# Optimization experiments

Measured on AMD Instinct MI355X. Metric: run time of the kernel, lower is better.

## Reference

```python
import jax, jax.numpy as jnp
import numpy as np

B, S, HID = 2, 2048, 2048
H, HK, D = 16, 4, 128  # num_heads, num_kv_heads, head_dim
G = H // HK            # GQA group size


def _make_rope(B, S, D):
    pos = jnp.arange(S, dtype=jnp.float32)
    inv_freq = 1.0 / (10000.0 ** (jnp.arange(0, D, 2, dtype=jnp.float32) / D))
    freqs = pos[:, None] * inv_freq[None, :]          # [S, D/2]
    emb = jnp.concatenate([freqs, freqs], axis=-1)     # [S, D]
    cos = jnp.broadcast_to(jnp.cos(emb)[None], (B, S, D))
    sin = jnp.broadcast_to(jnp.sin(emb)[None], (B, S, D))
    return cos, sin


def setup_inputs() -> dict:
    key = jax.random.key(0)
    k0, k1, k2 = jax.random.split(key, 3)
    hidden_states = jax.random.normal(k0, (B, S, HID), dtype=jnp.float32)
    cos, sin = _make_rope(B, S, D)
    w_qkv = jax.random.normal(k1, ((H + 2 * HK) * D, HID), dtype=jnp.float32) * 0.02
    b_qkv = jnp.zeros(((H + 2 * HK) * D,), dtype=jnp.float32)
    w_o = jax.random.normal(k2, (HID, HID), dtype=jnp.float32) * 0.02
    b_o = jnp.zeros((HID,), dtype=jnp.float32)
    return {"hidden_states": hidden_states, "cos": cos, "sin": sin,
            "w_qkv": w_qkv, "b_qkv": b_qkv, "w_o": w_o, "b_o": b_o}


def _rotate_half(x):
    x1, x2 = jnp.split(x, 2, axis=-1)
    return jnp.concatenate([-x2, x1], axis=-1)


def reference(hidden_states, cos, sin, w_qkv, b_qkv, w_o, b_o):
    b, s, _ = hidden_states.shape
    qkv = jnp.einsum('bsh,oh->bso', hidden_states, w_qkv) + b_qkv
    q, k, v = jnp.split(qkv, [H * D, (H + HK) * D], axis=-1)
    # [B, heads, S, D]
    q = q.reshape(b, s, H, D).transpose(0, 2, 1, 3)
    k = k.reshape(b, s, HK, D).transpose(0, 2, 1, 3)
    v = v.reshape(b, s, HK, D).transpose(0, 2, 1, 3)
    # RoPE (cos/sin broadcast over head axis)
    c = cos[:, None, :, :]
    sn = sin[:, None, :, :]
    q = q * c + _rotate_half(q) * sn
    k = k * c + _rotate_half(k) * sn
    # GQA attention without materializing repeated K/V: group q heads
    qg = q.reshape(b, HK, G, s, D)
    scale = 1.0 / jnp.sqrt(jnp.float32(D))
    scores = jnp.einsum('bkgqd,bkpd->bkgqp', qg, k) * scale  # [B,HK,G,S,S]
    probs = jax.nn.softmax(scores, axis=-1)
    out = jnp.einsum('bkgqp,bkpd->bkgqd', probs, v)           # [B,HK,G,S,D]
    out = out.reshape(b, H, s, D).transpose(0, 2, 1, 3).reshape(b, s, H * D)
    return jnp.einsum('bsh,oh->bso', out, w_o) + b_o
```

## Files before the change

kernel.cpp:

```cpp
#include <hip/hip_runtime.h>
#include <hip/hip_bf16.h>
#include <stdint.h>

typedef __bf16 bf16x8 __attribute__((ext_vector_type(8)));
typedef float f32x4 __attribute__((ext_vector_type(4)));
typedef float f32x16 __attribute__((ext_vector_type(16)));
typedef float f32x4v __attribute__((ext_vector_type(4)));
typedef unsigned short u16;
typedef unsigned int u32;
typedef u16 u16x8 __attribute__((ext_vector_type(8)));
typedef u32 u32x4 __attribute__((ext_vector_type(4)));

#define B_ 2
#define S_ 2048
#define HID_ 2048
#define H_ 16
#define HK_ 4
#define D_ 128
#define NQKV_ 3072

__device__ __forceinline__ u16 f2bf(float f) {
  u32 u = __builtin_bit_cast(u32, f);
  u32 r = (u + 0x7fffu + ((u >> 16) & 1u)) >> 16;
  return (u16)r;
}
__device__ __forceinline__ float bf2f(u16 v) {
  u32 u = ((u32)v) << 16;
  return __builtin_bit_cast(float, u);
}
__device__ __forceinline__ u32 cvtpk(float lo, float hi) {
  u32 r;
  asm("v_cvt_pk_bf16_f32 %0, %1, %2" : "=v"(r) : "v"(lo), "v"(hi));
  return r;
}
__device__ __forceinline__ void gload_lds16(const void* g, void* l) {
  __builtin_amdgcn_global_load_lds((const __attribute__((address_space(1))) void*)g,
                                   (__attribute__((address_space(3))) void*)l, 16, 0, 0);
}

__global__ __launch_bounds__(256) void k_cvt3(const float* __restrict__ a, u16* __restrict__ oa, int na,
                                              const float* __restrict__ b, u16* __restrict__ ob, int nb,
                                              const float* __restrict__ c, u16* __restrict__ oc, int nc) {
  int total = na + nb + nc;
  for (int i = blockIdx.x * 256 + threadIdx.x; i < total; i += gridDim.x * 256) {
    const float* src;
    u16* dst;
    int j = i;
    if (j < na) { src = a; dst = oa; }
    else if (j < na + nb) { j -= na; src = b; dst = ob; }
    else { j -= na + nb; src = c; dst = oc; }
    const f32x4v* p = (const f32x4v*)(src + (size_t)j * 8);
    f32x4v x = p[0], y = p[1];
    u16x8 w;
    w[0] = f2bf(x[0]); w[1] = f2bf(x[1]); w[2] = f2bf(x[2]); w[3] = f2bf(x[3]);
    w[4] = f2bf(y[0]); w[5] = f2bf(y[1]); w[6] = f2bf(y[2]); w[7] = f2bf(y[3]);
    *(u16x8*)(dst + (size_t)j * 8) = w;
  }
}

template <int ISSUES>
__device__ __forceinline__ void stage_half(const u16* __restrict__ src, int K, char* ldsb, int tid) {
#pragma unroll
  for (int i = 0; i < ISSUES; ++i) {
    int off = i * 8192 + tid * 16;
    int r = off >> 7, cb = off & 127;
    int scb = cb ^ ((r & 7) << 4);
    gload_lds16((const char*)(src + (size_t)r * K) + scb, ldsb + i * 8192 + (tid & ~63) * 16);
  }
}

template <int BM, typename CT>
__global__ __launch_bounds__(512, 1) void k_gemm8p(const u16* __restrict__ A, const u16* __restrict__ Bm,
                                                   const float* __restrict__ bias, CT* __restrict__ C,
                                                   int M, int N, int K) {
  constexpr int HAR = BM / 2;
  constexpr int AHB = HAR * 128;
  constexpr int AISS = AHB / 8192;
  constexpr int MREP = BM / 32;
  constexpr int MQ = MREP / 4;
  constexpr int DB = 2 * AHB + 32768;
  __shared__ __attribute__((aligned(16))) char lds[2 * DB];
  const int tid = threadIdx.x, lane = tid & 63;
  const int wid = tid >> 6, wm = wid >> 2, wn = wid & 3;
  const int l15 = lane & 15, l4 = lane >> 4;
  const int nwg = gridDim.x * gridDim.y;
  const int bid = blockIdx.y * gridDim.x + blockIdx.x;
  const int wgid = (bid & 7) * (nwg >> 3) + (bid >> 3);
  const int bx = wgid % gridDim.x, by = wgid / gridDim.x;
  const int row0 = by * BM, col0 = bx * 256;
  const int NT = K >> 6;

  f32x4 acc[MREP][4] = {};

  auto stageA = [&](int t, int h) {
    stage_half<AISS>(A + (size_t)(row0 + h * HAR) * K + t * 64, K, lds + (t & 1) * DB + h * AHB, tid);
  };
  auto stageB = [&](int t, int h) {
    stage_half<2>(Bm + (size_t)(col0 + h * 128) * K + t * 64, K, lds + (t & 1) * DB + 2 * AHB + h * 16384, tid);
  };

  stageA(0, 0); stageA(0, 1); stageB(0, 0); stageB(0, 1);
  if (NT > 1) { stageB(1, 0); stageB(1, 1); }
  if (NT > 1) asm volatile("s_waitcnt vmcnt(4)" ::: "memory");
  else        asm volatile("s_waitcnt vmcnt(0)" ::: "memory");
  __builtin_amdgcn_s_barrier();

  const char* myA = lds + wm * AHB;
  const char* myB = lds + 2 * AHB + (wn >> 1) * 16384;
  const int rBb = (wn & 1) * 64;

  for (int t = 0; t < NT; ++t) {
    const int d = t & 1;
    const char* Ab = myA + d * DB;
    const char* Bb = myB + d * DB;
    bf16x8 bfr[4][2];
#pragma unroll
    for (int j = 0; j < 4; ++j) {
      if (j == 0) {
#pragma unroll
        for (int n = 0; n < 4; ++n)
#pragma unroll
          for (int ks = 0; ks < 2; ++ks) {
            int r = rBb + n * 16 + l15;
            bfr[n][ks] = *(const bf16x8*)(Bb + r * 128 + ((ks * 64 + l4 * 16) ^ ((r & 7) << 4)));
          }
      }
      bf16x8 afr[MQ][2];
#pragma unroll
      for (int mq = 0; mq < MQ; ++mq)
#pragma unroll
        for (int ks = 0; ks < 2; ++ks) {
          int r = (j * MQ + mq) * 16 + l15;
          afr[mq][ks] = *(const bf16x8*)(Ab + r * 128 + ((ks * 64 + l4 * 16) ^ ((r & 7) << 4)));
        }
      if (j == 0) { if (t + 1 < NT) stageA(t + 1, 0); }
      else if (j == 1) { if (t + 1 < NT) stageA(t + 1, 1); }
      else if (j == 2) { if (t + 2 < NT) stageB(t + 2, 0); }
      else {
        if (t + 2 < NT) { stageB(t + 2, 1); asm volatile("s_waitcnt vmcnt(4)" ::: "memory"); }
        else             asm volatile("s_waitcnt vmcnt(0)" ::: "memory");
      }
      __builtin_amdgcn_s_barrier();
      asm volatile("s_waitcnt lgkmcnt(0)" ::: "memory");
      __builtin_amdgcn_s_setprio(1);
#pragma unroll
      for (int mq = 0; mq < MQ; ++mq)
#pragma unroll
        for (int ks = 0; ks < 2; ++ks)
#pragma unroll
          for (int n = 0; n < 4; ++n)
            acc[j * MQ + mq][n] =
                __builtin_amdgcn_mfma_f32_16x16x32_bf16(afr[mq][ks], bfr[n][ks], acc[j * MQ + mq][n], 0, 0, 0);
      __builtin_amdgcn_s_setprio(0);
      __builtin_amdgcn_s_barrier();
    }
  }

#pragma unroll
  for (int m = 0; m < MREP; ++m) {
    int grow = row0 + wm * HAR + m * 16 + l4 * 4;
#pragma unroll
    for (int n = 0; n < 4; ++n) {
      int gcol = col0 + wn * 64 + n * 16 + l15;
      float bv = bias[gcol];
#pragma unroll
      for (int r2 = 0; r2 < 4; ++r2) {
        float v = acc[m][n][r2] + bv;
        if constexpr (sizeof(CT) == 2) C[(size_t)(grow + r2) * N + gcol] = (CT)f2bf(v);
        else                           C[(size_t)(grow + r2) * N + gcol] = v;
      }
    }
  }
}

__global__ __launch_bounds__(256) void k_rope_split(const u16* __restrict__ qkv,
                                                    const float* __restrict__ cosb,
                                                    const float* __restrict__ sinb,
                                                    u16* __restrict__ Qb, u16* __restrict__ Kb,
                                                    u16* __restrict__ Vt) {
  const int bs = blockIdx.x;
  const int b = bs >> 11, s = bs & 2047;
  const size_t base = (size_t)bs * NQKV_;
  const size_t cs = (size_t)bs * D_;
  const int tid = threadIdx.x;
  const float qscale = 0.08838834764831845f;

  if (tid < 160) {
    const bool isq = tid < 128;
    const int idx = isq ? tid : (tid - 128);
    const int hh = idx >> 3, d0 = (idx & 7) * 8;
    const size_t srcb = base + (isq ? 0 : H_ * D_) + hh * D_;
    bf16x8 x1 = *(const bf16x8*)(qkv + srcb + d0);
    bf16x8 x2 = *(const bf16x8*)(qkv + srcb + d0 + 64);
    u16x8 y1, y2;
    const u16x8 u1 = __builtin_bit_cast(u16x8, x1);
    const u16x8 u2 = __builtin_bit_cast(u16x8, x2);
    const float sc = isq ? qscale : 1.0f;
#pragma unroll
    for (int i = 0; i < 8; ++i) {
      float f1 = bf2f(u1[i]), f2 = bf2f(u2[i]);
      float c1 = cosb[cs + d0 + i], s1 = sinb[cs + d0 + i];
      float c2 = cosb[cs + 64 + d0 + i], s2 = sinb[cs + 64 + d0 + i];
      y1[i] = f2bf((f1 * c1 - f2 * s1) * sc);
      y2[i] = f2bf((f2 * c2 + f1 * s2) * sc);
    }
    size_t o;
    if (isq) o = ((size_t)(b * H_ + hh) * S_ + s) * D_ + d0;
    else     o = ((size_t)(b * HK_ + hh) * S_ + s) * D_ + d0;
    u16* dst = isq ? Qb : Kb;
    *(u16x8*)(dst + o) = y1;
    *(u16x8*)(dst + o + 64) = y2;
  } else if (tid < 224) {
    const int idx = tid - 160;
    const int hk = idx >> 4, d0 = (idx & 15) * 8;
    bf16x8 xv = *(const bf16x8*)(qkv + base + (H_ + HK_) * D_ + hk * D_ + d0);
    const u16x8 uv = __builtin_bit_cast(u16x8, xv);
    u16* vb = Vt + (size_t)(b * HK_ + hk) * D_ * S_ + s;
#pragma unroll
    for (int i = 0; i < 8; ++i) vb[(size_t)(d0 + i) * S_] = uv[i];
  }
}

__global__ __launch_bounds__(512, 2) void k_attn(const u16* __restrict__ Qb, const u16* __restrict__ Kb,
                                                 const u16* __restrict__ Vt, u16* __restrict__ Ob) {
  __shared__ __attribute__((aligned(16))) char lds[65536];
  const int qt = blockIdx.x;
  const int bh = blockIdx.y;
  const int b = bh >> 4, h = bh & 15, hk = h >> 2;
  const int tid = threadIdx.x, lane = tid & 63, wid = tid >> 6;
  const int l31 = lane & 31, hi = lane >> 5;

  const int qrow = qt * 256 + wid * 32 + l31;
  const u16* qptr = Qb + ((size_t)(b * H_ + h) * S_ + qrow) * D_;
  bf16x8 qf[8];
#pragma unroll
  for (int ks = 0; ks < 8; ++ks) qf[ks] = *(const bf16x8*)(qptr + ks * 16 + hi * 8);

  const u16* kbase = Kb + (size_t)(b * HK_ + hk) * S_ * D_;
  const u16* vbase = Vt + (size_t)(b * HK_ + hk) * D_ * S_;

  int krow[2], kc[2], vrow[2], vc[2];
#pragma unroll
  for (int i = 0; i < 2; ++i) {
    int s = tid + i * 512;
    krow[i] = s >> 4; kc[i] = s & 15;
    vrow[i] = s >> 3; vc[i] = s & 7;
  }

  f32x16 o[4] = {};
  float mrun = -1e30f, lrun = 0.f;

  bf16x8 kreg[2], vreg[2];
#pragma unroll
  for (int i = 0; i < 2; ++i) {
    kreg[i] = *(const bf16x8*)(kbase + (size_t)krow[i] * D_ + kc[i] * 8);
    vreg[i] = *(const bf16x8*)(vbase + (size_t)vrow[i] * S_ + vc[i] * 8);
  }
#pragma unroll
  for (int i = 0; i < 2; ++i) {
    *(bf16x8*)(lds + ((krow[i] * 256 + kc[i] * 16) ^ ((krow[i] & 15) << 4))) = kreg[i];
    *(bf16x8*)(lds + 16384 + ((vrow[i] * 128 + vc[i] * 16) ^ ((vrow[i] & 7) << 4))) = vreg[i];
  }
  __syncthreads();

  for (int kt = 0; kt < 32; ++kt) {
    const int cur = kt & 1;
    const char* lKc = lds + cur * 32768;
    const char* lVc = lKc + 16384;

    if (kt < 31) {
#pragma unroll
      for (int i = 0; i < 2; ++i) {
        kreg[i] = *(const bf16x8*)(kbase + (size_t)((kt + 1) * 64 + krow[i]) * D_ + kc[i] * 8);
        vreg[i] = *(const bf16x8*)(vbase + (size_t)vrow[i] * S_ + (kt + 1) * 64 + vc[i] * 8);
      }
    }

    f32x16 sc[2] = {};
    __builtin_amdgcn_s_setprio(1);
#pragma unroll
    for (int ks = 0; ks < 8; ++ks) {
#pragma unroll
      for (int T = 0; T < 2; ++T) {
        int row = T * 32 + l31;
        bf16x8 kf = *(const bf16x8*)(lKc + ((row * 256 + ks * 32 + hi * 16) ^ ((row & 15) << 4)));
        sc[T] = __builtin_amdgcn_mfma_f32_32x32x16_bf16(kf, qf[ks], sc[T], 0, 0, 0);
      }
    }
    __builtin_amdgcn_s_setprio(0);

    float pmax = sc[0][0];
#pragma unroll
    for (int r = 1; r < 16; ++r) pmax = fmaxf(pmax, sc[0][r]);
#pragma unroll
    for (int r = 0; r < 16; ++r) pmax = fmaxf(pmax, sc[1][r]);
    pmax = fmaxf(pmax, __shfl_xor(pmax, 32));
    if (__any(pmax > mrun + 8.f)) {
      float mn = fmaxf(mrun, pmax);
      float alpha = __expf(mrun - mn);
      mrun = mn;
      lrun *= alpha;
#pragma unroll
      for (int dt = 0; dt < 4; ++dt)
#pragma unroll
        for (int r = 0; r < 16; ++r) o[dt][r] *= alpha;
    }
    float rs = 0.f;
#pragma unroll
    for (int T = 0; T < 2; ++T)
#pragma unroll
      for (int r = 0; r < 16; ++r) {
        float p = __expf(sc[T][r] - mrun);
        sc[T][r] = p;
        rs += p;
      }
    rs += __shfl_xor(rs, 32);
    lrun += rs;

    bf16x8 pf[4];
#pragma unroll
    for (int T = 0; T < 2; ++T) {
#pragma unroll
      for (int g = 0; g < 2; ++g) {
        u32 a0 = cvtpk(sc[T][8 * g + 0], sc[T][8 * g + 1]);
        u32 a1 = cvtpk(sc[T][8 * g + 2], sc[T][8 * g + 3]);
        u32 a2 = cvtpk(sc[T][8 * g + 4], sc[T][8 * g + 5]);
        u32 a3 = cvtpk(sc[T][8 * g + 6], sc[T][8 * g + 7]);
        u32 x0 = (u32)__shfl_xor((int)a0, 32);
        u32 x1 = (u32)__shfl_xor((int)a1, 32);
        u32 x2 = (u32)__shfl_xor((int)a2, 32);
        u32 x3 = (u32)__shfl_xor((int)a3, 32);
        u32 s0 = hi ? x2 : a0;
        u32 s1 = hi ? x3 : a1;
        u32 s2 = hi ? a2 : x0;
        u32 s3 = hi ? a3 : x1;
        u32x4 w = {s0, s1, s2, s3};
        pf[T * 2 + g] = __builtin_bit_cast(bf16x8, w);
      }
    }

    __builtin_amdgcn_s_setprio(1);
#pragma unroll
    for (int ks2 = 0; ks2 < 4; ++ks2) {
#pragma unroll
      for (int dt = 0; dt < 4; ++dt) {
        int row = dt * 32 + l31;
        bf16x8 vf = *(const bf16x8*)(lVc + ((row * 128 + ks2 * 32 + hi * 16) ^ ((row & 7) << 4)));
        o[dt] = __builtin_amdgcn_mfma_f32_32x32x16_bf16(vf, pf[ks2], o[dt], 0, 0, 0);
      }
    }
    __builtin_amdgcn_s_setprio(0);

    if (kt < 31) {
      char* nK = lds + (cur ^ 1) * 32768;
      char* nV = nK + 16384;
#pragma unroll
      for (int i = 0; i < 2; ++i) {
        *(bf16x8*)(nK + ((krow[i] * 256 + kc[i] * 16) ^ ((krow[i] & 15) << 4))) = kreg[i];
        *(bf16x8*)(nV + ((vrow[i] * 128 + vc[i] * 16) ^ ((vrow[i] & 7) << 4))) = vreg[i];
      }
    }
    __syncthreads();
  }

  float inv = 1.0f / lrun;
  char* myreg = lds + wid * 8192;
#pragma unroll
  for (int dt = 0; dt < 4; ++dt)
#pragma unroll
    for (int t = 0; t < 8; ++t) {
      u32 w = cvtpk(o[dt][2 * t] * inv, o[dt][2 * t + 1] * inv);
      int d0 = dt * 32 + 2 * (t & 1) + 8 * (t >> 1) + 4 * hi;
      *(u32*)(myreg + ((l31 * 256 + d0 * 2) ^ ((l31 & 15) << 4))) = w;
    }
  asm volatile("s_waitcnt lgkmcnt(0)");
  {
    int q = lane >> 1, hf = lane & 1;
    int srow = qt * 256 + wid * 32 + q;
    u16* orow = Ob + ((size_t)(b * S_ + srow)) * HID_ + h * 128 + hf * 64;
#pragma unroll
    for (int i = 0; i < 8; ++i) {
      bf16x8 vv = *(const bf16x8*)(myreg + ((q * 256 + hf * 128 + i * 16) ^ ((q & 15) << 4)));
      *(bf16x8*)(orow + i * 8) = vv;
    }
  }
}

extern "C" void kernel_launch(void* const* d_in, const int* in_sizes, int n_in,
                              void* d_out, int out_size, void* d_ws, size_t ws_size,
                              hipStream_t stream) {
  const float* hs = (const float*)d_in[0];
  const float* cosb = (const float*)d_in[1];
  const float* sinb = (const float*)d_in[2];
  const float* w_qkv = (const float*)d_in[3];
  const float* b_qkv = (const float*)d_in[4];
  const float* w_o = (const float*)d_in[5];
  const float* b_o = (const float*)d_in[6];
  float* out = (float*)d_out;

  char* ws = (char*)d_ws;
  u16* Xb    = (u16*)ws;
  u16* Wqkvb = (u16*)(ws + 16777216);
  u16* Wob   = (u16*)(ws + 29360128);
  u16* qkvb  = (u16*)(ws + 37748736);
  u16* Qb    = (u16*)(ws + 62914560);
  u16* Kb    = (u16*)(ws + 79691776);
  u16* Vt    = (u16*)(ws + 83886080);
  u16* Ob = Xb;

  hipLaunchKernelGGL(k_cvt3, dim3(2048), dim3(256), 0, stream,
                     hs, Xb, (B_ * S_ * HID_) / 8,
                     w_qkv, Wqkvb, (NQKV_ * HID_) / 8,
                     w_o, Wob, (HID_ * HID_) / 8);
  hipLaunchKernelGGL((k_gemm8p<256, u16>), dim3(NQKV_ / 256, (B_ * S_) / 256), dim3(512), 0, stream,
                     Xb, Wqkvb, b_qkv, qkvb, B_ * S_, NQKV_, HID_);
  hipLaunchKernelGGL(k_rope_split, dim3(B_ * S_), dim3(256), 0, stream, qkvb, cosb, sinb, Qb, Kb, Vt);
  hipLaunchKernelGGL(k_attn, dim3(S_ / 256, B_ * H_), dim3(512), 0, stream, Qb, Kb, Vt, Ob);
  hipLaunchKernelGGL((k_gemm8p<128, float>), dim3(HID_ / 256, (B_ * S_) / 128), dim3(512), 0, stream,
                     Ob, Wob, b_o, out, B_ * S_, HID_, HID_);
}
```

Baseline: 217.6 us.

## Split attention KV sequence across two wave groups and merge partial softmax states

Each attention block now covers 128 query rows instead of 256, and its two groups of four waves each process half of the KV sequence. The partial outputs and running max/sum are combined through LDS at the end. K/V tiles are loaded directly into LDS with gload_lds16 instead of going through registers. This doubles the grid (512 blocks) for better CU occupancy, but each group is now single-buffered, adds two barriers per iteration, and adds an LDS merge step.

```diff
diff --git a/kernel.cpp b/kernel.cpp
--- a/kernel.cpp
+++ b/kernel.cpp
@@ -223,59 +223,51 @@
 
 __global__ __launch_bounds__(512, 2) void k_attn(const u16* __restrict__ Qb, const u16* __restrict__ Kb,
                                                  const u16* __restrict__ Vt, u16* __restrict__ Ob) {
-  __shared__ __attribute__((aligned(16))) char lds[65536];
+  __shared__ __attribute__((aligned(16))) char lds[66560];
   const int qt = blockIdx.x;
   const int bh = blockIdx.y;
   const int b = bh >> 4, h = bh & 15, hk = h >> 2;
   const int tid = threadIdx.x, lane = tid & 63, wid = tid >> 6;
   const int l31 = lane & 31, hi = lane >> 5;
-
-  const int qrow = qt * 256 + wid * 32 + l31;
+  const int g = wid >> 2, wq = wid & 3;
+
+  const int qrow = qt * 128 + wq * 32 + l31;
   const u16* qptr = Qb + ((size_t)(b * H_ + h) * S_ + qrow) * D_;
   bf16x8 qf[8];
 #pragma unroll
   for (int ks = 0; ks < 8; ++ks) qf[ks] = *(const bf16x8*)(qptr + ks * 16 + hi * 8);
 
-  const u16* kbase = Kb + (size_t)(b * HK_ + hk) * S_ * D_;
-  const u16* vbase = Vt + (size_t)(b * HK_ + hk) * D_ * S_;
-
-  int krow[2], kc[2], vrow[2], vc[2];
-#pragma unroll
-  for (int i = 0; i < 2; ++i) {
-    int s = tid + i * 512;
-    krow[i] = s >> 4; kc[i] = s & 15;
-    vrow[i] = s >> 3; vc[i] = s & 7;
-  }
+  const char* kB = (const char*)(Kb + (size_t)(b * HK_ + hk) * S_ * D_);
+  const char* vB = (const char*)(Vt + (size_t)(b * HK_ + hk) * D_ * S_);
+  char* gbase = lds + g * 32768;
+
+  int koff[4], voff[4];
+#pragma unroll
+  for (int i = 0; i < 4; ++i) {
+    int c = wq * 256 + i * 64 + lane;
+    int row = c >> 4, u = c & 15;
+    koff[i] = row * 256 + ((u ^ (row & 15)) << 4);
+    int d = c >> 3, uv = c & 7;
+    voff[i] = d * (S_ * 2) + ((uv ^ (d & 7)) << 4);
+  }
+
+  auto stage = [&](int tt) {
+#pragma unroll
+    for (int i = 0; i < 4; ++i)
+      gload_lds16(kB + (size_t)tt * 16384 + koff[i], gbase + wq * 4096 + i * 1024);
+#pragma unroll
+    for (int i = 0; i < 4; ++i)
+      gload_lds16(vB + (size_t)tt * 128 + voff[i], gbase + 16384 + wq * 4096 + i * 1024);
+  };
 
   f32x16 o[4] = {};
   float mrun = -1e30f, lrun = 0.f;
 
-  bf16x8 kreg[2], vreg[2];
-#pragma unroll
-  for (int i = 0; i < 2; ++i) {
-    kreg[i] = *(const bf16x8*)(kbase + (size_t)krow[i] * D_ + kc[i] * 8);
-    vreg[i] = *(const bf16x8*)(vbase + (size_t)vrow[i] * S_ + vc[i] * 8);
-  }
-#pragma unroll
-  for (int i = 0; i < 2; ++i) {
-    *(bf16x8*)(lds + ((krow[i] * 256 + kc[i] * 16) ^ ((krow[i] & 15) << 4))) = kreg[i];
-    *(bf16x8*)(lds + 16384 + ((vrow[i] * 128 + vc[i] * 16) ^ ((vrow[i] & 7) << 4))) = vreg[i];
-  }
+  const int tt0 = g * 16;
+  stage(tt0);
   __syncthreads();
 
-  for (int kt = 0; kt < 32; ++kt) {
-    const int cur = kt & 1;
-    const char* lKc = lds + cur * 32768;
-    const char* lVc = lKc + 16384;
-
-    if (kt < 31) {
-#pragma unroll
-      for (int i = 0; i < 2; ++i) {
-        kreg[i] = *(const bf16x8*)(kbase + (size_t)((kt + 1) * 64 + krow[i]) * D_ + kc[i] * 8);
-        vreg[i] = *(const bf16x8*)(vbase + (size_t)vrow[i] * S_ + (kt + 1) * 64 + vc[i] * 8);
-      }
-    }
-
+  for (int t = 0; t < 16; ++t) {
     f32x16 sc[2] = {};
     __builtin_amdgcn_s_setprio(1);
 #pragma unroll
@@ -283,7 +275,7 @@
 #pragma unroll
       for (int T = 0; T < 2; ++T) {
         int row = T * 32 + l31;
-        bf16x8 kf = *(const bf16x8*)(lKc + ((row * 256 + ks * 32 + hi * 16) ^ ((row & 15) << 4)));
+        bf16x8 kf = *(const bf16x8*)(gbase + ((row * 256 + ks * 32 + hi * 16) ^ ((row & 15) << 4)));
         sc[T] = __builtin_amdgcn_mfma_f32_32x32x16_bf16(kf, qf[ks], sc[T], 0, 0, 0);
       }
     }
@@ -321,11 +313,11 @@
 #pragma unroll
     for (int T = 0; T < 2; ++T) {
 #pragma unroll
-      for (int g = 0; g < 2; ++g) {
-        u32 a0 = cvtpk(sc[T][8 * g + 0], sc[T][8 * g + 1]);
-        u32 a1 = cvtpk(sc[T][8 * g + 2], sc[T][8 * g + 3]);
-        u32 a2 = cvtpk(sc[T][8 * g + 4], sc[T][8 * g + 5]);
-        u32 a3 = cvtpk(sc[T][8 * g + 6], sc[T][8 * g + 7]);
+      for (int gg = 0; gg < 2; ++gg) {
+        u32 a0 = cvtpk(sc[T][8 * gg + 0], sc[T][8 * gg + 1]);
+        u32 a1 = cvtpk(sc[T][8 * gg + 2], sc[T][8 * gg + 3]);
+        u32 a2 = cvtpk(sc[T][8 * gg + 4], sc[T][8 * gg + 5]);
+        u32 a3 = cvtpk(sc[T][8 * gg + 6], sc[T][8 * gg + 7]);
         u32 x0 = (u32)__shfl_xor((int)a0, 32);
         u32 x1 = (u32)__shfl_xor((int)a1, 32);
         u32 x2 = (u32)__shfl_xor((int)a2, 32);
@@ -335,7 +327,7 @@
         u32 s2 = hi ? a2 : x0;
         u32 s3 = hi ? a3 : x1;
         u32x4 w = {s0, s1, s2, s3};
-        pf[T * 2 + g] = __builtin_bit_cast(bf16x8, w);
+        pf[T * 2 + gg] = __builtin_bit_cast(bf16x8, w);
       }
     }
 
@@ -345,43 +337,69 @@
 #pragma unroll
       for (int dt = 0; dt < 4; ++dt) {
         int row = dt * 32 + l31;
-        bf16x8 vf = *(const bf16x8*)(lVc + ((row * 128 + ks2 * 32 + hi * 16) ^ ((row & 7) << 4)));
+        bf16x8 vf = *(const bf16x8*)(gbase + 16384 + ((row * 128 + ks2 * 32 + hi * 16) ^ ((row & 7) << 4)));
         o[dt] = __builtin_amdgcn_mfma_f32_32x32x16_bf16(vf, pf[ks2], o[dt], 0, 0, 0);
       }
     }
     __builtin_amdgcn_s_setprio(0);
 
-    if (kt < 31) {
-      char* nK = lds + (cur ^ 1) * 32768;
-      char* nV = nK + 16384;
-#pragma unroll
-      for (int i = 0; i < 2; ++i) {
-        *(bf16x8*)(nK + ((krow[i] * 256 + kc[i] * 16) ^ ((krow[i] & 15) << 4))) = kreg[i];
-        *(bf16x8*)(nV + ((vrow[i] * 128 + vc[i] * 16) ^ ((vrow[i] & 7) << 4))) = vreg[i];
-      }
-    }
     __syncthreads();
-  }
-
-  float inv = 1.0f / lrun;
-  char* myreg = lds + wid * 8192;
-#pragma unroll
-  for (int dt = 0; dt < 4; ++dt)
-#pragma unroll
-    for (int t = 0; t < 8; ++t) {
-      u32 w = cvtpk(o[dt][2 * t] * inv, o[dt][2 * t + 1] * inv);
-      int d0 = dt * 32 + 2 * (t & 1) + 8 * (t >> 1) + 4 * hi;
-      *(u32*)(myreg + ((l31 * 256 + d0 * 2) ^ ((l31 & 15) << 4))) = w;
-    }
-  asm volatile("s_waitcnt lgkmcnt(0)");
-  {
-    int q = lane >> 1, hf = lane & 1;
-    int srow = qt * 256 + wid * 32 + q;
-    u16* orow = Ob + ((size_t)(b * S_ + srow)) * HID_ + h * 128 + hf * 64;
-#pragma unroll
-    for (int i = 0; i < 8; ++i) {
-      bf16x8 vv = *(const bf16x8*)(myreg + ((q * 256 + hf * 128 + i * 16) ^ ((q & 15) << 4)));
-      *(bf16x8*)(orow + i * 8) = vv;
+    if (t < 15) stage(tt0 + t + 1);
+    __syncthreads();
+  }
+
+  float2* mlb = (float2*)(lds + 65536);
+  if (g == 1) {
+    char* ob = lds + wq * 16384;
+#pragma unroll
+    for (int dt = 0; dt < 4; ++dt)
+#pragma unroll
+      for (int r = 0; r < 4; ++r) {
+        f32x4 w = {o[dt][4 * r + 0], o[dt][4 * r + 1], o[dt][4 * r + 2], o[dt][4 * r + 3]};
+        *(f32x4*)(ob + ((size_t)((dt * 4 + r) * 64 + lane)) * 16) = w;
+      }
+    if (!hi) mlb[wq * 32 + l31] = float2{mrun, lrun};
+  }
+  __syncthreads();
+  float inv = 0.f;
+  if (g == 0) {
+    float2 ml1 = mlb[wq * 32 + l31];
+    float m = fmaxf(mrun, ml1.x);
+    float a0 = __expf(mrun - m), a1 = __expf(ml1.x - m);
+    float lt = lrun * a0 + ml1.y * a1;
+    char* ob = lds + wq * 16384;
+#pragma unroll
+    for (int dt = 0; dt < 4; ++dt)
+#pragma unroll
+      for (int r = 0; r < 4; ++r) {
+        f32x4 c1 = *(const f32x4*)(ob + ((size_t)((dt * 4 + r) * 64 + lane)) * 16);
+#pragma unroll
+        for (int j = 0; j < 4; ++j) o[dt][4 * r + j] = o[dt][4 * r + j] * a0 + c1[j] * a1;
+      }
+    inv = 1.0f / lt;
+  }
+  __syncthreads();
+
+  if (g == 0) {
+    char* myreg = lds + wq * 8192;
+#pragma unroll
+    for (int dt = 0; dt < 4; ++dt)
+#pragma unroll
+      for (int t = 0; t < 8; ++t) {
+        u32 w = cvtpk(o[dt][2 * t] * inv, o[dt][2 * t + 1] * inv);
+        int d0 = dt * 32 + 2 * (t & 1) + 8 * (t >> 1) + 4 * hi;
+        *(u32*)(myreg + ((l31 * 256 + d0 * 2) ^ ((l31 & 15) << 4))) = w;
+      }
+    asm volatile("s_waitcnt lgkmcnt(0)");
+    {
+      int q = lane >> 1, hf = lane & 1;
+      int srow = qt * 128 + wq * 32 + q;
+      u16* orow = Ob + ((size_t)(b * S_ + srow)) * HID_ + h * 128 + hf * 64;
+#pragma unroll
+      for (int i = 0; i < 8; ++i) {
+        bf16x8 vv = *(const bf16x8*)(myreg + ((q * 256 + hf * 128 + i * 16) ^ ((q & 15) << 4)));
+        *(bf16x8*)(orow + i * 8) = vv;
+      }
     }
   }
 }
@@ -415,7 +433,7 @@
   hipLaunchKernelGGL((k_gemm8p<256, u16>), dim3(NQKV_ / 256, (B_ * S_) / 256), dim3(512), 0, stream,
                      Xb, Wqkvb, b_qkv, qkvb, B_ * S_, NQKV_, HID_);
   hipLaunchKernelGGL(k_rope_split, dim3(B_ * S_), dim3(256), 0, stream, qkvb, cosb, sinb, Qb, Kb, Vt);
-  hipLaunchKernelGGL(k_attn, dim3(S_ / 256, B_ * H_), dim3(512), 0, stream, Qb, Kb, Vt, Ob);
+  hipLaunchKernelGGL(k_attn, dim3(S_ / 128, B_ * H_), dim3(512), 0, stream, Qb, Kb, Vt, Ob);
   hipLaunchKernelGGL((k_gemm8p<128, float>), dim3(HID_ / 256, (B_ * S_) / 128), dim3(512), 0, stream,
                      Ob, Wob, b_o, out, B_ * S_, HID_, HID_);
 }
```

Measured after the change: 232.0 us. 1.07x slower.

## Fuse RoPE and Q/K split into QKV GEMM epilogue via LDS staging

Applied to the files above, without the earlier changes.

The QKV GEMM epilogue for the Q and K column tiles now stages accumulator rows through LDS, applies bias, RoPE and the Q scale, and writes Q and K directly in head-major bf16 layout. The separate rope/split kernel is replaced by a small kernel that only transposes V. This removes a round trip of Q/K through the intermediate qkv buffer and one full pass over it. In exchange it adds extra barriers and serialized LDS exchange in the GEMM epilogue, and the new V kernel uses scalar strided stores.

```diff
diff --git a/kernel.cpp b/kernel.cpp
--- a/kernel.cpp
+++ b/kernel.cpp
@@ -69,10 +69,13 @@
   }
 }
 
-template <int BM, typename CT>
+template <int BM, typename CT, bool FUSE>
 __global__ __launch_bounds__(512, 1) void k_gemm8p(const u16* __restrict__ A, const u16* __restrict__ Bm,
                                                    const float* __restrict__ bias, CT* __restrict__ C,
-                                                   int M, int N, int K) {
+                                                   int M, int N, int K,
+                                                   const float* __restrict__ cosb,
+                                                   const float* __restrict__ sinb,
+                                                   u16* __restrict__ Qp, u16* __restrict__ Kp) {
   constexpr int HAR = BM / 2;
   constexpr int AHB = HAR * 128;
   constexpr int AISS = AHB / 8192;
@@ -156,68 +159,81 @@
     }
   }
 
-#pragma unroll
-  for (int m = 0; m < MREP; ++m) {
-    int grow = row0 + wm * HAR + m * 16 + l4 * 4;
-#pragma unroll
-    for (int n = 0; n < 4; ++n) {
-      int gcol = col0 + wn * 64 + n * 16 + l15;
-      float bv = bias[gcol];
-#pragma unroll
-      for (int r2 = 0; r2 < 4; ++r2) {
-        float v = acc[m][n][r2] + bv;
-        if constexpr (sizeof(CT) == 2) C[(size_t)(grow + r2) * N + gcol] = (CT)f2bf(v);
-        else                           C[(size_t)(grow + r2) * N + gcol] = v;
-      }
-    }
-  }
-}
-
-__global__ __launch_bounds__(256) void k_rope_split(const u16* __restrict__ qkv,
-                                                    const float* __restrict__ cosb,
-                                                    const float* __restrict__ sinb,
-                                                    u16* __restrict__ Qb, u16* __restrict__ Kb,
-                                                    u16* __restrict__ Vt) {
+  bool fusedQK = false;
+  if constexpr (FUSE) fusedQK = (col0 < (H_ + HK_) * D_);
+  if (fusedQK) {
+    float* ex = (float*)lds;
+    const int hg0 = col0 >> 7;
+    const bool isq = hg0 < H_;
+    const float rsc = isq ? 0.08838834764831845f : 1.0f;
+    u16* dstb = isq ? Qp : Kp;
+    const int hbase = isq ? hg0 : (hg0 - H_);
+    const int HN = isq ? H_ : HK_;
+    const int r = tid >> 4, p = tid & 15;
+    const int hh = p >> 3, d0 = (p & 7) * 8;
+    const int rr = r & 15, wmr = r >> 4;
+#pragma unroll 1
+    for (int m = 0; m < MREP; ++m) {
+#pragma unroll
+      for (int n = 0; n < 4; ++n) {
+        int colw = wn * 64 + n * 16 + l15;
+        float bv = bias[col0 + colw];
+#pragma unroll
+        for (int r2 = 0; r2 < 4; ++r2)
+          ex[(wm * 16 + l4 * 4 + r2) * 264 + colw] = acc[m][n][r2] + bv;
+      }
+      __syncthreads();
+      {
+        int grow = row0 + wmr * 128 + m * 16 + rr;
+        int bb = grow >> 11, ss = grow & 2047;
+        size_t cs = ((size_t)bb * S_ + ss) * D_;
+        const float* exr = ex + (wmr * 16 + rr) * 264 + hh * 128;
+        f32x4 lo0 = *(const f32x4*)(exr + d0);
+        f32x4 lo1 = *(const f32x4*)(exr + d0 + 4);
+        f32x4 hi0 = *(const f32x4*)(exr + 64 + d0);
+        f32x4 hi1 = *(const f32x4*)(exr + 64 + d0 + 4);
+        u16x8 y1, y2;
+#pragma unroll
+        for (int i = 0; i < 8; ++i) {
+          float lo = (i < 4) ? lo0[i] : lo1[i - 4];
+          float hi2 = (i < 4) ? hi0[i] : hi1[i - 4];
+          float c1 = cosb[cs + d0 + i], s1 = sinb[cs + d0 + i];
+          float c2 = cosb[cs + 64 + d0 + i], s2 = sinb[cs + 64 + d0 + i];
+          y1[i] = f2bf((lo * c1 - hi2 * s1) * rsc);
+          y2[i] = f2bf((hi2 * c2 + lo * s2) * rsc);
+        }
+        u16* drow = dstb + (((size_t)(bb * HN + hbase + hh)) * S_ + ss) * D_;
+        *(u16x8*)(drow + d0) = y1;
+        *(u16x8*)(drow + d0 + 64) = y2;
+      }
+      __syncthreads();
+    }
+  } else {
+#pragma unroll
+    for (int m = 0; m < MREP; ++m) {
+      int grow = row0 + wm * HAR + m * 16 + l4 * 4;
+#pragma unroll
+      for (int n = 0; n < 4; ++n) {
+        int gcol = col0 + wn * 64 + n * 16 + l15;
+        float bv = bias[gcol];
+#pragma unroll
+        for (int r2 = 0; r2 < 4; ++r2) {
+          float v = acc[m][n][r2] + bv;
+          if constexpr (sizeof(CT) == 2) C[(size_t)(grow + r2) * N + gcol] = (CT)f2bf(v);
+          else                           C[(size_t)(grow + r2) * N + gcol] = v;
+        }
+      }
+    }
+  }
+}
+
+__global__ __launch_bounds__(128) void k_vsplit(const u16* __restrict__ qkv, u16* __restrict__ Vt) {
   const int bs = blockIdx.x;
   const int b = bs >> 11, s = bs & 2047;
-  const size_t base = (size_t)bs * NQKV_;
-  const size_t cs = (size_t)bs * D_;
-  const int tid = threadIdx.x;
-  const float qscale = 0.08838834764831845f;
-
-  if (tid < 160) {
-    const bool isq = tid < 128;
-    const int idx = isq ? tid : (tid - 128);
-    const int hh = idx >> 3, d0 = (idx & 7) * 8;
-    const size_t srcb = base + (isq ? 0 : H_ * D_) + hh * D_;
-    bf16x8 x1 = *(const bf16x8*)(qkv + srcb + d0);
-    bf16x8 x2 = *(const bf16x8*)(qkv + srcb + d0 + 64);
-    u16x8 y1, y2;
-    const u16x8 u1 = __builtin_bit_cast(u16x8, x1);
-    const u16x8 u2 = __builtin_bit_cast(u16x8, x2);
-    const float sc = isq ? qscale : 1.0f;
-#pragma unroll
-    for (int i = 0; i < 8; ++i) {
-      float f1 = bf2f(u1[i]), f2 = bf2f(u2[i]);
-      float c1 = cosb[cs + d0 + i], s1 = sinb[cs + d0 + i];
-      float c2 = cosb[cs + 64 + d0 + i], s2 = sinb[cs + 64 + d0 + i];
-      y1[i] = f2bf((f1 * c1 - f2 * s1) * sc);
-      y2[i] = f2bf((f2 * c2 + f1 * s2) * sc);
-    }
-    size_t o;
-    if (isq) o = ((size_t)(b * H_ + hh) * S_ + s) * D_ + d0;
-    else     o = ((size_t)(b * HK_ + hh) * S_ + s) * D_ + d0;
-    u16* dst = isq ? Qb : Kb;
-    *(u16x8*)(dst + o) = y1;
-    *(u16x8*)(dst + o + 64) = y2;
-  } else if (tid < 224) {
-    const int idx = tid - 160;
-    const int hk = idx >> 4, d0 = (idx & 15) * 8;
-    bf16x8 xv = *(const bf16x8*)(qkv + base + (H_ + HK_) * D_ + hk * D_ + d0);
-    const u16x8 uv = __builtin_bit_cast(u16x8, xv);
-    u16* vb = Vt + (size_t)(b * HK_ + hk) * D_ * S_ + s;
-#pragma unroll
-    for (int i = 0; i < 8; ++i) vb[(size_t)(d0 + i) * S_] = uv[i];
+  const u16* src = qkv + (size_t)bs * NQKV_ + (H_ + HK_) * D_;
+  for (int j = threadIdx.x; j < HK_ * D_; j += 128) {
+    int hk = j >> 7, d = j & 127;
+    Vt[((size_t)(b * HK_ + hk) * D_ + d) * S_ + s] = src[j];
   }
 }
 
@@ -412,10 +428,10 @@
                      hs, Xb, (B_ * S_ * HID_) / 8,
                      w_qkv, Wqkvb, (NQKV_ * HID_) / 8,
                      w_o, Wob, (HID_ * HID_) / 8);
-  hipLaunchKernelGGL((k_gemm8p<256, u16>), dim3(NQKV_ / 256, (B_ * S_) / 256), dim3(512), 0, stream,
-                     Xb, Wqkvb, b_qkv, qkvb, B_ * S_, NQKV_, HID_);
-  hipLaunchKernelGGL(k_rope_split, dim3(B_ * S_), dim3(256), 0, stream, qkvb, cosb, sinb, Qb, Kb, Vt);
+  hipLaunchKernelGGL((k_gemm8p<256, u16, true>), dim3(NQKV_ / 256, (B_ * S_) / 256), dim3(512), 0, stream,
+                     Xb, Wqkvb, b_qkv, qkvb, B_ * S_, NQKV_, HID_, cosb, sinb, Qb, Kb);
+  hipLaunchKernelGGL(k_vsplit, dim3(B_ * S_), dim3(128), 0, stream, qkvb, Vt);
   hipLaunchKernelGGL(k_attn, dim3(S_ / 256, B_ * H_), dim3(512), 0, stream, Qb, Kb, Vt, Ob);
-  hipLaunchKernelGGL((k_gemm8p<128, float>), dim3(HID_ / 256, (B_ * S_) / 128), dim3(512), 0, stream,
-                     Ob, Wob, b_o, out, B_ * S_, HID_, HID_);
-}
+  hipLaunchKernelGGL((k_gemm8p<128, float, false>), dim3(HID_ / 256, (B_ * S_) / 128), dim3(512), 0, stream,
+                     Ob, Wob, b_o, out, B_ * S_, HID_, HID_, nullptr, nullptr, nullptr, nullptr);
+}
```

Result: slower. 241.1 us (+10.8%).
